# Kernel optimization log

Hardware: AMD Instinct MI355X
Metric: run time of the kernel (lower is better)

The kernel has to match this reference:

```python
import jax, jax.numpy as jnp
import numpy as np

NFPS = 10

def setup_inputs() -> dict:
    key = jax.random.key(0)
    k1, k2, k3, k4 = jax.random.split(key, 4)
    B, D_IN, H, D_OUT = 131072, 2 * NFPS * 3, 256, NFPS * 3 * 12
    x = jax.random.normal(k1, (B, D_IN), dtype=jnp.float32)
    centres = jax.random.normal(k2, (H, D_IN), dtype=jnp.float32)
    sigmas = jax.random.uniform(k3, (H,), dtype=jnp.float32)
    W2 = jax.random.normal(k4, (D_OUT, H), dtype=jnp.float32) * (1.0 / np.sqrt(H))
    return {"x": x, "centres": centres, "sigmas": sigmas, "W2": W2}

def reference(x, centres, sigmas, W2):
    # RBF layer: distances = ||x - c|| * sigma; gaussian: exp(-distances^2)
    x2 = jnp.sum(x * x, axis=-1, keepdims=True)            # [B,1]
    c2 = jnp.sum(centres * centres, axis=-1)               # [H]
    xc = jnp.einsum('bd,hd->bh', x, centres)               # [B,H]
    d2 = jnp.maximum(x2 + c2[None, :] - 2.0 * xc, 0.0)     # squared distance, clamp fp noise
    phi = jnp.exp(-(sigmas[None, :] ** 2) * d2)            # [B,H]
    out = jnp.einsum('bh,oh->bo', phi, W2)                 # [B, nFPs*3*12]
    B = x.shape[0]
    out = out.reshape(B, NFPS, 12, 3).transpose(0, 1, 3, 2).reshape(B, 3 * NFPS, 12)
    return out
```

## Files before the change

kernel.cpp:

```cpp
#include <hip/hip_runtime.h>

#define THREADS 512
#define DIN 60
#define HN 256
#define DOUT 360

typedef __attribute__((ext_vector_type(8))) short short8;
typedef __attribute__((ext_vector_type(16))) float f32x16;
typedef __attribute__((ext_vector_type(4))) float f32x4;
typedef __attribute__((ext_vector_type(4))) unsigned int u32x4;

#define WS_CBF   0
#define WS_W2    32768

__device__ __forceinline__ short bf16_bits(float f) {
    union { float f; unsigned u; } v; v.f = f;
    unsigned r = (v.u + 0x7FFFu + ((v.u >> 16) & 1u)) >> 16;
    return (short)(unsigned short)r;
}

__device__ __forceinline__ unsigned pk_bf16(float a, float b) {
    unsigned r;
    asm("v_cvt_pk_bf16_f32 %0, %1, %2" : "=v"(r) : "v"(a), "v"(b));
    return r;
}

__device__ __forceinline__ void gload16(const void* g, void* lds) {
    __builtin_amdgcn_global_load_lds(
        (const __attribute__((address_space(1))) unsigned int*)(uintptr_t)g,
        (__attribute__((address_space(3))) unsigned int*)(unsigned int)(uintptr_t)lds,
        16, 0, 0);
}

__global__ void prep(const float* __restrict__ centres, const float* __restrict__ sigmas,
                     const float* __restrict__ W2, short* __restrict__ ws)
{
    int t = blockIdx.x * 256 + threadIdx.x;
    if (t < 12288) {
        int row = t >> 5, pc = t & 31;
        int c = pc ^ (row & 31);
        short8 v = {0,0,0,0,0,0,0,0};
        if (row < DOUT) {
            int rr = row / 12, jj = row % 12;
            int fcl = rr / 3, kk = rr % 3;
            int o = fcl * 36 + jj * 3 + kk;
            const float* src = W2 + o * HN + c * 8;
            #pragma unroll
            for (int i = 0; i < 8; ++i) v[i] = bf16_bits(src[i]);
        }
        *(short8*)(ws + (WS_W2 / 2) + t * 8) = v;
    } else if (t < 14336) {
        int j = t - 12288;
        int row = j >> 3, p = j & 7;
        int c = p ^ (row & 7);
        const float* cr = centres + row * DIN;
        float sg = sigmas[row];
        union { unsigned u; float f; } nq;
        nq.u = ((unsigned)(unsigned short)bf16_bits(2.f * sg * sg * 1.44269504088896340736f)) << 16;
        const float nsq = nq.f;
        short8 v = {0,0,0,0,0,0,0,0};
        if (c < 7) {
            #pragma unroll
            for (int i = 0; i < 8; ++i) {
                int k = c * 8 + i;
                if (k < DIN) v[i] = bf16_bits(nsq * cr[k]);
            }
        } else {
            #pragma unroll
            for (int i = 0; i < 4; ++i) v[i] = bf16_bits(nsq * cr[56 + i]);
            float c2 = 0.f;
            #pragma unroll
            for (int d = 0; d < DIN; ++d) c2 = fmaf(cr[d], cr[d], c2);
            float T = -0.5f * nsq * c2;
            union { unsigned u; float f; } th;
            th.u = ((unsigned)(unsigned short)bf16_bits(T)) << 16;
            v[4] = bf16_bits(th.f);
            v[5] = bf16_bits(T - th.f);
            v[6] = bf16_bits(-0.5f * nsq);
            v[7] = v[6];
        }
        *(short8*)(ws + (WS_CBF / 2) + j * 8) = v;
    }
}

__device__ __forceinline__ void load_xtile(const float* __restrict__ x, int row0,
                                           int l31, int hi, short8 xb[4]) {
    const float* xr = x + (size_t)(row0 + l31) * DIN;
    f32x4 xa[4][2];
    #pragma unroll
    for (int kt = 0; kt < 4; ++kt) {
        int k0 = kt * 16 + hi * 8;
        xa[kt][0] = *(const f32x4*)(xr + k0);
        xa[kt][1] = (k0 + 4 < DIN) ? *(const f32x4*)(xr + k0 + 4) : (f32x4){0.f,0.f,0.f,0.f};
    }
    float p2 = 0.f;
    #pragma unroll
    for (int kt = 0; kt < 4; ++kt)
        #pragma unroll
        for (int h = 0; h < 2; ++h)
            #pragma unroll
            for (int i = 0; i < 4; ++i) p2 = fmaf(xa[kt][h][i], xa[kt][h][i], p2);
    float x2v = p2 + __shfl_xor(p2, 32);
    union { unsigned u; float f; } hb; hb.u = pk_bf16(x2v, 0.f) << 16;
    float x2lo = x2v - hb.f;
    #pragma unroll
    for (int kt = 0; kt < 4; ++kt) {
        union { u32x4 u; short8 s; } a;
        a.u[0] = pk_bf16(xa[kt][0][0], xa[kt][0][1]);
        a.u[1] = pk_bf16(xa[kt][0][2], xa[kt][0][3]);
        a.u[2] = pk_bf16(xa[kt][1][0], xa[kt][1][1]);
        a.u[3] = pk_bf16(xa[kt][1][2], xa[kt][1][3]);
        if (kt == 3) {
            a.u[2] = hi ? 0x3F803F80u : a.u[2];
            a.u[3] = hi ? pk_bf16(hb.f, x2lo) : a.u[3];
        }
        xb[kt] = a.s;
    }
}

__global__ __launch_bounds__(THREADS, 2)
void rbf_main(const float* __restrict__ x, const short* __restrict__ ws,
              float* __restrict__ out)
{
    __shared__ short8 w2h[6144];
    __shared__ short8 cbf[2048];

    const int tid  = threadIdx.x;
    const int w    = tid >> 6;
    const int lane = tid & 63;
    const int l31  = lane & 31;
    const int hi   = lane >> 5;
    const int bid  = blockIdx.x;
    const int f     = (bid >> 3) & 1;
    const int sbase = (bid & 7) | ((bid >> 4) << 3);

    #pragma unroll
    for (int i = 0; i < 12; ++i)
        gload16(ws + (WS_W2 / 2) + ((size_t)f * 6144 + i * THREADS + tid) * 8,
                (char*)w2h + (i * THREADS + tid) * 16);
    #pragma unroll
    for (int i = 0; i < 4; ++i)
        gload16(ws + (WS_CBF / 2) + (i * THREADS + tid) * 8, (char*)cbf + (i * THREADS + tid) * 16);

    short8 xb[4];
    load_xtile(x, sbase * 1024 + w * 32, l31, hi, xb);

    __syncthreads();

    for (int it = 0; it < 4; ++it) {
        const int rb = sbase * 1024 + it * 256 + w * 32;

        f32x16 acc2[6];
        #pragma unroll
        for (int nt = 0; nt < 6; ++nt) acc2[nt] = (f32x16){};

        #pragma unroll
        for (int nt1 = 0; nt1 < 8; ++nt1) {
            f32x16 a1 = (f32x16){};
            const int row = nt1 * 32 + l31;
            __builtin_amdgcn_s_setprio(1);
            #pragma unroll
            for (int kt = 0; kt < 4; ++kt) {
                short8 cf = cbf[row * 8 + ((kt * 2 + hi) ^ (row & 7))];
                a1 = __builtin_amdgcn_mfma_f32_32x32x16_bf16(cf, xb[kt], a1, 0, 0, 0);
            }
            __builtin_amdgcn_s_setprio(0);

            unsigned pwl[4][2];
            #pragma unroll
            for (int q = 0; q < 4; ++q) {
                float ph[4];
                #pragma unroll
                for (int j = 0; j < 4; ++j)
                    ph[j] = exp2f(fminf(a1[4 * q + j], 0.f));
                pwl[q][0] = pk_bf16(ph[0], ph[1]);
                pwl[q][1] = pk_bf16(ph[2], ph[3]);
            }

            #pragma unroll
            for (int m = 0; m < 2; ++m) {
                unsigned d0 = pwl[2 * m][0], s0 = pwl[2 * m + 1][0];
                unsigned d1 = pwl[2 * m][1], s1 = pwl[2 * m + 1][1];
                asm("v_permlane32_swap_b32 %0, %1" : "+v"(d0), "+v"(s0));
                asm("v_permlane32_swap_b32 %0, %1" : "+v"(d1), "+v"(s1));
                union { u32x4 u; short8 s; } bfr;
                bfr.u[0] = d0; bfr.u[1] = d1; bfr.u[2] = s0; bfr.u[3] = s1;
                const int ktg = nt1 * 2 + m;

                __builtin_amdgcn_s_setprio(1);
                #pragma unroll
                for (int nt = 0; nt < 6; ++nt) {
                    int lrow = nt * 32 + l31;
                    short8 wf = w2h[lrow * 32 + ((ktg * 2 + hi) ^ l31)];
                    acc2[nt] = __builtin_amdgcn_mfma_f32_32x32x16_bf16(wf, bfr.s, acc2[nt], 0, 0, 0);
                }
                __builtin_amdgcn_s_setprio(0);
            }
        }

        if (it < 3)
            load_xtile(x, rb + 256, l31, hi, xb);

        {
            float* op = out + (size_t)(rb + l31) * DOUT;
            #pragma unroll
            for (int nt = 0; nt < 6; ++nt) {
                #pragma unroll
                for (int q = 0; q < 4; ++q) {
                    int col = f * 192 + nt * 32 + q * 8 + hi * 4;
                    if (col < DOUT) {
                        f32x4 v;
                        v[0] = acc2[nt][4 * q + 0]; v[1] = acc2[nt][4 * q + 1];
                        v[2] = acc2[nt][4 * q + 2]; v[3] = acc2[nt][4 * q + 3];
                        *(f32x4*)(op + col) = v;
                    }
                }
            }
        }
    }
}

extern "C" void kernel_launch(void* const* d_in, const int* in_sizes, int n_in,
                              void* d_out, int out_size, void* d_ws, size_t ws_size,
                              hipStream_t stream) {
    const float* x       = (const float*)d_in[0];
    const float* centres = (const float*)d_in[1];
    const float* sigmas  = (const float*)d_in[2];
    const float* W2      = (const float*)d_in[3];
    float* out = (float*)d_out;
    short* ws  = (short*)d_ws;
    prep<<<dim3(56), dim3(256), 0, stream>>>(centres, sigmas, W2, ws);
    rbf_main<<<dim3(256), dim3(THREADS), 0, stream>>>(x, ws, out);
}
```

Measured before the change: 63.12 us.

## Halve block size and have each wave process two 32-row tiles sharing LDS fragments

Each block now runs 4 waves instead of 8, and each wave handles two 32-row batch tiles. Every centre and W2 fragment read from LDS then feeds two MFMAs, which halves LDS read traffic per MFMA and gives the scheduler two independent MFMA chains to interleave. The s_setprio hints are removed. In exchange, per-thread register use roughly doubles (two sets of 6 accumulators), occupancy drops to one block per CU with launch_bounds 1, and there are fewer waves to hide latency.

Result: slower. 75.18 us (+19.1%).

```diff
diff --git a/kernel.cpp b/kernel.cpp
--- a/kernel.cpp
+++ b/kernel.cpp
@@ -1,6 +1,6 @@
 #include <hip/hip_runtime.h>
 
-#define THREADS 512
+#define THREADS 256
 #define DIN 60
 #define HN 256
 #define DOUT 360
@@ -118,7 +118,7 @@
     }
 }
 
-__global__ __launch_bounds__(THREADS, 2)
+__global__ __launch_bounds__(THREADS, 1)
 void rbf_main(const float* __restrict__ x, const short* __restrict__ ws,
               float* __restrict__ out)
 {
@@ -135,74 +135,87 @@
     const int sbase = (bid & 7) | ((bid >> 4) << 3);
 
     #pragma unroll
-    for (int i = 0; i < 12; ++i)
+    for (int i = 0; i < 24; ++i)
         gload16(ws + (WS_W2 / 2) + ((size_t)f * 6144 + i * THREADS + tid) * 8,
                 (char*)w2h + (i * THREADS + tid) * 16);
     #pragma unroll
-    for (int i = 0; i < 4; ++i)
+    for (int i = 0; i < 8; ++i)
         gload16(ws + (WS_CBF / 2) + (i * THREADS + tid) * 8, (char*)cbf + (i * THREADS + tid) * 16);
 
-    short8 xb[4];
-    load_xtile(x, sbase * 1024 + w * 32, l31, hi, xb);
+    short8 xb0[4], xb1[4];
+    load_xtile(x, sbase * 1024 + w * 64,      l31, hi, xb0);
+    load_xtile(x, sbase * 1024 + w * 64 + 32, l31, hi, xb1);
 
     __syncthreads();
 
     for (int it = 0; it < 4; ++it) {
-        const int rb = sbase * 1024 + it * 256 + w * 32;
-
-        f32x16 acc2[6];
-        #pragma unroll
-        for (int nt = 0; nt < 6; ++nt) acc2[nt] = (f32x16){};
+        const int rb = sbase * 1024 + it * 256 + w * 64;
+
+        f32x16 acc2[2][6];
+        #pragma unroll
+        for (int t = 0; t < 2; ++t)
+            #pragma unroll
+            for (int nt = 0; nt < 6; ++nt) acc2[t][nt] = (f32x16){};
 
         #pragma unroll
         for (int nt1 = 0; nt1 < 8; ++nt1) {
-            f32x16 a1 = (f32x16){};
+            f32x16 a10 = (f32x16){}, a11 = (f32x16){};
             const int row = nt1 * 32 + l31;
-            __builtin_amdgcn_s_setprio(1);
             #pragma unroll
             for (int kt = 0; kt < 4; ++kt) {
                 short8 cf = cbf[row * 8 + ((kt * 2 + hi) ^ (row & 7))];
-                a1 = __builtin_amdgcn_mfma_f32_32x32x16_bf16(cf, xb[kt], a1, 0, 0, 0);
-            }
-            __builtin_amdgcn_s_setprio(0);
-
-            unsigned pwl[4][2];
+                a10 = __builtin_amdgcn_mfma_f32_32x32x16_bf16(cf, xb0[kt], a10, 0, 0, 0);
+                a11 = __builtin_amdgcn_mfma_f32_32x32x16_bf16(cf, xb1[kt], a11, 0, 0, 0);
+            }
+
+            unsigned pwl0[4][2], pwl1[4][2];
             #pragma unroll
             for (int q = 0; q < 4; ++q) {
-                float ph[4];
+                float p0[4], p1[4];
                 #pragma unroll
-                for (int j = 0; j < 4; ++j)
-                    ph[j] = exp2f(fminf(a1[4 * q + j], 0.f));
-                pwl[q][0] = pk_bf16(ph[0], ph[1]);
-                pwl[q][1] = pk_bf16(ph[2], ph[3]);
+                for (int j = 0; j < 4; ++j) {
+                    p0[j] = exp2f(fminf(a10[4 * q + j], 0.f));
+                    p1[j] = exp2f(fminf(a11[4 * q + j], 0.f));
+                }
+                pwl0[q][0] = pk_bf16(p0[0], p0[1]);
+                pwl0[q][1] = pk_bf16(p0[2], p0[3]);
+                pwl1[q][0] = pk_bf16(p1[0], p1[1]);
+                pwl1[q][1] = pk_bf16(p1[2], p1[3]);
             }
 
             #pragma unroll
             for (int m = 0; m < 2; ++m) {
-                unsigned d0 = pwl[2 * m][0], s0 = pwl[2 * m + 1][0];
-                unsigned d1 = pwl[2 * m][1], s1 = pwl[2 * m + 1][1];
-                asm("v_permlane32_swap_b32 %0, %1" : "+v"(d0), "+v"(s0));
-                asm("v_permlane32_swap_b32 %0, %1" : "+v"(d1), "+v"(s1));
-                union { u32x4 u; short8 s; } bfr;
-                bfr.u[0] = d0; bfr.u[1] = d1; bfr.u[2] = s0; bfr.u[3] = s1;
+                unsigned d00 = pwl0[2 * m][0], s00 = pwl0[2 * m + 1][0];
+                unsigned d01 = pwl0[2 * m][1], s01 = pwl0[2 * m + 1][1];
+                asm("v_permlane32_swap_b32 %0, %1" : "+v"(d00), "+v"(s00));
+                asm("v_permlane32_swap_b32 %0, %1" : "+v"(d01), "+v"(s01));
+                unsigned d10 = pwl1[2 * m][0], s10 = pwl1[2 * m + 1][0];
+                unsigned d11 = pwl1[2 * m][1], s11 = pwl1[2 * m + 1][1];
+                asm("v_permlane32_swap_b32 %0, %1" : "+v"(d10), "+v"(s10));
+                asm("v_permlane32_swap_b32 %0, %1" : "+v"(d11), "+v"(s11));
+                union { u32x4 u; short8 s; } b0, b1;
+                b0.u[0] = d00; b0.u[1] = d01; b0.u[2] = s00; b0.u[3] = s01;
+                b1.u[0] = d10; b1.u[1] = d11; b1.u[2] = s10; b1.u[3] = s11;
                 const int ktg = nt1 * 2 + m;
 
-                __builtin_amdgcn_s_setprio(1);
                 #pragma unroll
                 for (int nt = 0; nt < 6; ++nt) {
                     int lrow = nt * 32 + l31;
                     short8 wf = w2h[lrow * 32 + ((ktg * 2 + hi) ^ l31)];
-                    acc2[nt] = __builtin_amdgcn_mfma_f32_32x32x16_bf16(wf, bfr.s, acc2[nt], 0, 0, 0);
+                    acc2[0][nt] = __builtin_amdgcn_mfma_f32_32x32x16_bf16(wf, b0.s, acc2[0][nt], 0, 0, 0);
+                    acc2[1][nt] = __builtin_amdgcn_mfma_f32_32x32x16_bf16(wf, b1.s, acc2[1][nt], 0, 0, 0);
                 }
-                __builtin_amdgcn_s_setprio(0);
-            }
-        }
-
-        if (it < 3)
-            load_xtile(x, rb + 256, l31, hi, xb);
-
-        {
-            float* op = out + (size_t)(rb + l31) * DOUT;
+            }
+        }
+
+        if (it < 3) {
+            load_xtile(x, rb + 256,      l31, hi, xb0);
+            load_xtile(x, rb + 256 + 32, l31, hi, xb1);
+        }
+
+        #pragma unroll
+        for (int t = 0; t < 2; ++t) {
+            float* op = out + (size_t)(rb + t * 32 + l31) * DOUT;
             #pragma unroll
             for (int nt = 0; nt < 6; ++nt) {
                 #pragma unroll
@@ -210,8 +223,8 @@
                     int col = f * 192 + nt * 32 + q * 8 + hi * 4;
                     if (col < DOUT) {
                         f32x4 v;
-                        v[0] = acc2[nt][4 * q + 0]; v[1] = acc2[nt][4 * q + 1];
-                        v[2] = acc2[nt][4 * q + 2]; v[3] = acc2[nt][4 * q + 3];
+                        v[0] = acc2[t][nt][4 * q + 0]; v[1] = acc2[t][nt][4 * q + 1];
+                        v[2] = acc2[t][nt][4 * q + 2]; v[3] = acc2[t][nt][4 * q + 3];
                         *(f32x4*)(op + col) = v;
                     }
                 }
```
